# Performance work log

Hardware: AMD Instinct MI355X
Metric: run time of the kernel (lower is better)

## Reference

```python
import jax, jax.numpy as jnp
import numpy as np

N = 4096
IN_DIM = 128
OUT_DIM = 64
LEAKY_SLOPE = 0.2


def setup_inputs() -> dict:
    key = jax.random.key(0)
    ks = jax.random.split(key, 8)
    H = jax.random.normal(ks[0], (N, IN_DIM), dtype=jnp.float32)
    # dense 0/1 adjacency per relation (int constants w.r.t. autodiff)
    A_buys = jax.random.randint(ks[1], (N, N), 0, 2, dtype=jnp.int32)
    A_views = jax.random.randint(ks[2], (N, N), 0, 2, dtype=jnp.int32)
    # xavier_uniform for W (stored [in, out]; Wh = H @ W == torch Linear with weight W.T)
    s_w = float(np.sqrt(6.0 / (IN_DIM + OUT_DIM)))
    W_buys = jax.random.uniform(ks[3], (IN_DIM, OUT_DIM), jnp.float32, -s_w, s_w)
    W_views = jax.random.uniform(ks[4], (IN_DIM, OUT_DIM), jnp.float32, -s_w, s_w)
    # xavier_uniform on a.view(1, 2*out_dim)
    s_a = float(np.sqrt(6.0 / (1 + 2 * OUT_DIM)))
    a_buys = jax.random.uniform(ks[5], (2 * OUT_DIM,), jnp.float32, -s_a, s_a)
    a_views = jax.random.uniform(ks[6], (2 * OUT_DIM,), jnp.float32, -s_a, s_a)
    bias = jnp.zeros((OUT_DIM,), dtype=jnp.float32)
    return {"H": H, "A_buys": A_buys, "A_views": A_views,
            "W_buys": W_buys, "W_views": W_views,
            "a_buys": a_buys, "a_views": a_views, "bias": bias}


def _relation(H, A, W, a):
    Wh = H @ W                                  # [N, OUT]
    # (cat(Wh_i, Wh_j) * a).sum(-1) == Wh_i @ a[:OUT] + Wh_j @ a[OUT:]
    s_i = Wh @ a[:OUT_DIM]                      # [N]
    s_j = Wh @ a[OUT_DIM:]                      # [N]
    e = jax.nn.leaky_relu(s_i[:, None] + s_j[None, :], LEAKY_SLOPE)  # [N, N]
    e = jnp.where(A == 0, -jnp.inf, e)
    alpha = jnp.nan_to_num(jax.nn.softmax(e, axis=1))                # isolated rows -> 0
    return alpha @ Wh                           # [N, OUT]


def reference(H, A_buys, A_views, W_buys, W_views, a_buys, a_views, bias):
    agg = _relation(H, A_buys, W_buys, a_buys) + _relation(H, A_views, W_views, a_views)
    return agg + bias
```

## Files before the change

kernel.cpp:

```cpp
#include <hip/hip_runtime.h>

#define NN 4096
#define IND 128
#define OUTD 64
#define WJ 128
#define NWIN 8
#define LOG2E 1.44269504088896340736f

typedef __attribute__((ext_vector_type(4))) float  floatx4;
typedef __attribute__((ext_vector_type(8))) __bf16 bf16x8;
typedef __attribute__((ext_vector_type(4))) int    intx4;

#if __has_builtin(__builtin_amdgcn_exp2f)
#define EXP2(x) __builtin_amdgcn_exp2f(x)
#else
#define EXP2(x) exp2f(x)
#endif

__device__ __forceinline__ unsigned short f2bf(float f) {
  unsigned int u = __float_as_uint(f);
  u += 0x7fffu + ((u >> 16) & 1u);
  return (unsigned short)(u >> 16);
}

__global__ __launch_bounds__(256) void gat_prep(
    const float* __restrict__ H,
    const float* __restrict__ W0, const float* __restrict__ W1,
    const float* __restrict__ av0, const float* __restrict__ av1,
    unsigned short* __restrict__ whF,
    float* __restrict__ sA, float* __restrict__ sB)
{
  const int rel = blockIdx.y;
  const float* __restrict__ W  = rel ? W1 : W0;
  const float* __restrict__ av = rel ? av1 : av0;
  const int i0 = blockIdx.x * 16;
  const int t = threadIdx.x;
  const int c = t & 63;
  const int wv = __builtin_amdgcn_readfirstlane(t >> 6);
  const float* __restrict__ hp = H + (size_t)(i0 + wv * 4) * IND;

  float acc0 = 0.f, acc1 = 0.f, acc2 = 0.f, acc3 = 0.f;
#pragma unroll 8
  for (int k = 0; k < IND; k += 4) {
    float4 h0 = *(const float4*)(hp + k);
    float4 h1 = *(const float4*)(hp + IND + k);
    float4 h2 = *(const float4*)(hp + 2 * IND + k);
    float4 h3 = *(const float4*)(hp + 3 * IND + k);
    float w0 = W[(k + 0) * OUTD + c];
    float w1 = W[(k + 1) * OUTD + c];
    float w2 = W[(k + 2) * OUTD + c];
    float w3 = W[(k + 3) * OUTD + c];
    acc0 += h0.x * w0 + h0.y * w1 + h0.z * w2 + h0.w * w3;
    acc1 += h1.x * w0 + h1.y * w1 + h1.z * w2 + h1.w * w3;
    acc2 += h2.x * w0 + h2.y * w1 + h2.z * w2 + h2.w * w3;
    acc3 += h3.x * w0 + h3.y * w1 + h3.z * w2 + h3.w * w3;
  }

  const float alo = av[c] * LOG2E, ahi = av[OUTD + c] * LOG2E;
  float pa0 = acc0 * alo, pa1 = acc1 * alo, pa2 = acc2 * alo, pa3 = acc3 * alo;
  float pb0 = acc0 * ahi, pb1 = acc1 * ahi, pb2 = acc2 * ahi, pb3 = acc3 * ahi;
#pragma unroll
  for (int off = 32; off >= 1; off >>= 1) {
    pa0 += __shfl_xor(pa0, off); pa1 += __shfl_xor(pa1, off);
    pa2 += __shfl_xor(pa2, off); pa3 += __shfl_xor(pa3, off);
    pb0 += __shfl_xor(pb0, off); pb1 += __shfl_xor(pb1, off);
    pb2 += __shfl_xor(pb2, off); pb3 += __shfl_xor(pb3, off);
  }
  const int ibase = i0 + wv * 4;
  if (c == 0) {
    float* sa = sA + rel * NN + ibase;
    float* sb = sB + rel * NN + ibase;
    sa[0] = pa0; sa[1] = pa1; sa[2] = pa2; sa[3] = pa3;
    sb[0] = pb0; sb[1] = pb1; sb[2] = pb2; sb[3] = pb3;
  }

  unsigned long long packed =
      (unsigned long long)f2bf(acc0)        | ((unsigned long long)f2bf(acc1) << 16) |
      ((unsigned long long)f2bf(acc2) << 32) | ((unsigned long long)f2bf(acc3) << 48);
  *(unsigned long long*)(whF + ((size_t)(rel * 512 + (ibase >> 3)) * 64 + c) * 8 + (ibase & 7)) = packed;
}

__global__ __launch_bounds__(256, 2) void gat_fused(
    const int* __restrict__ A0, const int* __restrict__ A1,
    const unsigned short* __restrict__ whF,
    const float* __restrict__ sA, const float* __restrict__ sB,
    float* __restrict__ numer,
    float* __restrict__ denom)
{
  __shared__ char lds[4][2][4096];
  const int rel  = blockIdx.y;
  const int i0   = blockIdx.x * 16;
  const int t    = threadIdx.x;
  const int w    = t >> 6;
  const int lane = t & 63;
  const int quad = lane >> 4;
  const int m    = lane & 15;
  const int lj   = lane & 31;
  const int half = lane >> 5;
  const int s_st = lj >> 1;
  const int wboff = s_st * 256 + (lj & 1) * 8;
  const int* __restrict__ A = rel ? A1 : A0;
  const unsigned short* __restrict__ wh = whF + (size_t)rel * 512 * 64 * 8;
  const float* __restrict__ sbp = sB + rel * NN;

  const float siv = sA[rel * NN + i0 + m];
  const int jbase = w * (NWIN * WJ);

  floatx4 acc0 = {0.f,0.f,0.f,0.f}, acc1 = acc0, acc2 = acc0, acc3 = acc0, acc4 = acc0;
  bf16x8 vone;
#pragma unroll
  for (int k = 0; k < 8; k++) vone[k] = (__bf16)1.0f;

  intx4  av2[2][8];
  float4 sjv2[2];
  bf16x8 b[4][4];

  auto issueA = [&](int win) {
    const int jw = jbase + win * WJ;
    const int buf = win & 1;
    sjv2[buf] = *(const float4*)(sbp + jw + lj * 4);
    const int* pA = A + (size_t)(i0 + half) * NN + jw + lj * 4;
#pragma unroll
    for (int p = 0; p < 8; p++)
      av2[buf][p] = __builtin_nontemporal_load((const intx4*)(pA + (size_t)(2 * p) * NN));
  };

  auto stage = [&](int win) {
    const int buf = win & 1;
    char* slice = lds[w][buf];
    const float4 sjv = sjv2[buf];
#pragma unroll
    for (int p = 0; p < 8; p++) {
      const int rp = 2 * p + half;
      const float si = __shfl(siv, rp);
      float t0 = si + sjv.x, t1 = si + sjv.y, t2 = si + sjv.z, t3 = si + sjv.w;
      float e0 = EXP2(fmaxf(t0, 0.2f * t0));
      float e1 = EXP2(fmaxf(t1, 0.2f * t1));
      float e2 = EXP2(fmaxf(t2, 0.2f * t2));
      float e3 = EXP2(fmaxf(t3, 0.2f * t3));
      const intx4 a4 = av2[buf][p];
      e0 = a4[0] ? e0 : 0.f;
      e1 = a4[1] ? e1 : 0.f;
      e2 = a4[2] ? e2 : 0.f;
      e3 = a4[3] ? e3 : 0.f;
      uint2 pk;
      pk.x = (unsigned)f2bf(e0) | ((unsigned)f2bf(e1) << 16);
      pk.y = (unsigned)f2bf(e2) | ((unsigned)f2bf(e3) << 16);
      *(uint2*)(slice + wboff + ((rp ^ s_st) & 15) * 16) = pk;
    }
  };

  auto issueB = [&](int win) {
    const int jw = jbase + win * WJ;
    const unsigned short* bb = wh + ((size_t)(jw >> 3) + quad) * 512 + (size_t)m * 8;
#pragma unroll
    for (int ks = 0; ks < 4; ks++)
#pragma unroll
      for (int nt = 0; nt < 4; nt++)
        b[ks][nt] = *(const bf16x8*)(bb + (size_t)ks * 2048 + nt * 128);
  };

  auto domfma = [&](int win) {
    char* slice = lds[w][win & 1];
    bf16x8 afr[4];
#pragma unroll
    for (int ks = 0; ks < 4; ks++) {
      const int s = ks * 4 + quad;
      afr[ks] = *(const bf16x8*)(slice + s * 256 + ((m ^ s) & 15) * 16);
    }
#pragma unroll
    for (int ks = 0; ks < 4; ks++) {
      acc0 = __builtin_amdgcn_mfma_f32_16x16x32_bf16(afr[ks], b[ks][0], acc0, 0, 0, 0);
      acc1 = __builtin_amdgcn_mfma_f32_16x16x32_bf16(afr[ks], b[ks][1], acc1, 0, 0, 0);
      acc2 = __builtin_amdgcn_mfma_f32_16x16x32_bf16(afr[ks], b[ks][2], acc2, 0, 0, 0);
      acc3 = __builtin_amdgcn_mfma_f32_16x16x32_bf16(afr[ks], b[ks][3], acc3, 0, 0, 0);
      acc4 = __builtin_amdgcn_mfma_f32_16x16x32_bf16(afr[ks], vone,     acc4, 0, 0, 0);
    }
  };

  issueA(0);
  stage(0);
  issueA(1);

#pragma unroll
  for (int win = 0; win < NWIN; win++) {
    issueB(win);
    if (win + 2 < NWIN) issueA(win + 2);
    if (win + 1 < NWIN) stage(win + 1);
    domfma(win);
  }

  float* redw  = (float*)lds[w][0];
  float* dredw = (float*)lds[w][1];
#pragma unroll
  for (int r = 0; r < 4; r++) {
    const int row = quad * 4 + r;
    redw[row * 64 + 0 * 16 + m] = acc0[r];
    redw[row * 64 + 1 * 16 + m] = acc1[r];
    redw[row * 64 + 2 * 16 + m] = acc2[r];
    redw[row * 64 + 3 * 16 + m] = acc3[r];
  }
  if (m == 0) {
#pragma unroll
    for (int r = 0; r < 4; r++) dredw[quad * 4 + r] = acc4[r];
  }
  __syncthreads();

  const int c  = t & 63;
  const int r0 = t >> 6;
  const size_t base = (size_t)rel * NN;
#pragma unroll
  for (int rr = r0; rr < 16; rr += 4) {
    float nsum = 0.f, ds = 0.f;
#pragma unroll
    for (int ww = 0; ww < 4; ww++) {
      nsum += ((const float*)lds[ww][0])[rr * 64 + c];
      ds   += ((const float*)lds[ww][1])[rr];
    }
    numer[(base + i0 + rr) * OUTD + c] = nsum;
    if (c == 0) denom[base + i0 + rr] = ds;
  }
}

__global__ __launch_bounds__(256) void gat_combine(
    const float* __restrict__ numer, const float* __restrict__ denom,
    const float* __restrict__ bias, float* __restrict__ out)
{
  const int idx = blockIdx.x * 256 + threadIdx.x;
  const int i  = idx >> 4;
  const int c4 = idx & 15;
  const float4* nv = (const float4*)numer;

  float4 o = ((const float4*)bias)[c4];
#pragma unroll
  for (int rel = 0; rel < 2; rel++) {
    const size_t base = (size_t)rel * NN + i;
    float4 n = nv[base * 16 + c4];
    float  d = denom[base];
    float inv = d > 0.f ? 1.f / d : 0.f;
    o.x += n.x * inv; o.y += n.y * inv; o.z += n.z * inv; o.w += n.w * inv;
  }
  ((float4*)out)[idx] = o;
}

extern "C" void kernel_launch(void* const* d_in, const int* in_sizes, int n_in,
                              void* d_out, int out_size, void* d_ws, size_t ws_size,
                              hipStream_t stream) {
  const float* H    = (const float*)d_in[0];
  const int*   A0   = (const int*)d_in[1];
  const int*   A1   = (const int*)d_in[2];
  const float* W0   = (const float*)d_in[3];
  const float* W1   = (const float*)d_in[4];
  const float* av0  = (const float*)d_in[5];
  const float* av1  = (const float*)d_in[6];
  const float* bias = (const float*)d_in[7];
  float* out = (float*)d_out;

  const size_t whF_b = (size_t)2 * 512 * 64 * 8 * 2;
  const size_t s_b   = (size_t)2 * NN * 4;

  unsigned short* whF   = (unsigned short*)d_ws;
  float*          sA    = (float*)((char*)d_ws + whF_b);
  float*          sB    = (float*)((char*)d_ws + whF_b + s_b);
  float*          numer = (float*)((char*)d_ws + whF_b + 2 * s_b);
  float*          denom = numer + (size_t)2 * NN * OUTD;

  gat_prep<<<dim3(NN / 16, 2), 256, 0, stream>>>(H, W0, W1, av0, av1, whF, sA, sB);
  gat_fused<<<dim3(NN / 16, 2), 256, 0, stream>>>(A0, A1, whF, sA, sB, numer, denom);
  gat_combine<<<(NN * OUTD / 4) / 256, 256, 0, stream>>>(numer, denom, bias, out);
}
```

Measured before the change: 178.9 us.

## Cut register pressure: bitmask adjacency, split B fragment loads, raise occupancy

Raises the launch bound from 2 to 4 blocks per SIMD. To fit that, it compresses the prefetched adjacency vectors into a 32-bit bitmask per window instead of holding two windows of int4 registers. It also halves the B-fragment register buffer by loading and issuing the MFMAs in two k-halves. The aim is higher occupancy to hide global-memory latency. The cost is less prefetch lookahead for B, extra bit-pack instructions, and possible spills if the tighter register cap is not met.

```diff
diff --git a/kernel.cpp b/kernel.cpp
--- a/kernel.cpp
+++ b/kernel.cpp
@@ -80,7 +80,7 @@
   *(unsigned long long*)(whF + ((size_t)(rel * 512 + (ibase >> 3)) * 64 + c) * 8 + (ibase & 7)) = packed;
 }
 
-__global__ __launch_bounds__(256, 2) void gat_fused(
+__global__ __launch_bounds__(256, 4) void gat_fused(
     const int* __restrict__ A0, const int* __restrict__ A1,
     const unsigned short* __restrict__ whF,
     const float* __restrict__ sA, const float* __restrict__ sB,
@@ -111,38 +111,51 @@
 #pragma unroll
   for (int k = 0; k < 8; k++) vone[k] = (__bf16)1.0f;
 
-  intx4  av2[2][8];
-  float4 sjv2[2];
-  bf16x8 b[4][4];
+  intx4    atr[8];
+  unsigned maskw[2];
+  float4   sjv2[2];
+  bf16x8   b[2][4];
 
   auto issueA = [&](int win) {
     const int jw = jbase + win * WJ;
-    const int buf = win & 1;
-    sjv2[buf] = *(const float4*)(sbp + jw + lj * 4);
+    sjv2[win & 1] = *(const float4*)(sbp + jw + lj * 4);
     const int* pA = A + (size_t)(i0 + half) * NN + jw + lj * 4;
 #pragma unroll
     for (int p = 0; p < 8; p++)
-      av2[buf][p] = __builtin_nontemporal_load((const intx4*)(pA + (size_t)(2 * p) * NN));
+      atr[p] = __builtin_nontemporal_load((const intx4*)(pA + (size_t)(2 * p) * NN));
+  };
+
+  auto packA = [&](int win) {
+    unsigned mk = 0;
+#pragma unroll
+    for (int p = 0; p < 8; p++) {
+      mk |= (atr[p][0] ? 1u : 0u) << (4 * p);
+      mk |= (atr[p][1] ? 2u : 0u) << (4 * p);
+      mk |= (atr[p][2] ? 4u : 0u) << (4 * p);
+      mk |= (atr[p][3] ? 8u : 0u) << (4 * p);
+    }
+    maskw[win & 1] = mk;
   };
 
   auto stage = [&](int win) {
     const int buf = win & 1;
     char* slice = lds[w][buf];
     const float4 sjv = sjv2[buf];
+    const unsigned mk = maskw[buf];
 #pragma unroll
     for (int p = 0; p < 8; p++) {
       const int rp = 2 * p + half;
       const float si = __shfl(siv, rp);
+      const unsigned nib = mk >> (4 * p);
       float t0 = si + sjv.x, t1 = si + sjv.y, t2 = si + sjv.z, t3 = si + sjv.w;
       float e0 = EXP2(fmaxf(t0, 0.2f * t0));
       float e1 = EXP2(fmaxf(t1, 0.2f * t1));
       float e2 = EXP2(fmaxf(t2, 0.2f * t2));
       float e3 = EXP2(fmaxf(t3, 0.2f * t3));
-      const intx4 a4 = av2[buf][p];
-      e0 = a4[0] ? e0 : 0.f;
-      e1 = a4[1] ? e1 : 0.f;
-      e2 = a4[2] ? e2 : 0.f;
-      e3 = a4[3] ? e3 : 0.f;
+      e0 = (nib & 1u) ? e0 : 0.f;
+      e1 = (nib & 2u) ? e1 : 0.f;
+      e2 = (nib & 4u) ? e2 : 0.f;
+      e3 = (nib & 8u) ? e3 : 0.f;
       uint2 pk;
       pk.x = (unsigned)f2bf(e0) | ((unsigned)f2bf(e1) << 16);
       pk.y = (unsigned)f2bf(e2) | ((unsigned)f2bf(e3) << 16);
@@ -150,44 +163,46 @@
     }
   };
 
-  auto issueB = [&](int win) {
+  auto issueB = [&](int win, int h) {
     const int jw = jbase + win * WJ;
     const unsigned short* bb = wh + ((size_t)(jw >> 3) + quad) * 512 + (size_t)m * 8;
 #pragma unroll
-    for (int ks = 0; ks < 4; ks++)
+    for (int k2 = 0; k2 < 2; k2++)
 #pragma unroll
       for (int nt = 0; nt < 4; nt++)
-        b[ks][nt] = *(const bf16x8*)(bb + (size_t)ks * 2048 + nt * 128);
-  };
-
-  auto domfma = [&](int win) {
+        b[k2][nt] = *(const bf16x8*)(bb + (size_t)(2 * h + k2) * 2048 + nt * 128);
+  };
+
+  auto domfma = [&](int win, int h) {
     char* slice = lds[w][win & 1];
-    bf16x8 afr[4];
-#pragma unroll
-    for (int ks = 0; ks < 4; ks++) {
-      const int s = ks * 4 + quad;
-      afr[ks] = *(const bf16x8*)(slice + s * 256 + ((m ^ s) & 15) * 16);
-    }
-#pragma unroll
-    for (int ks = 0; ks < 4; ks++) {
-      acc0 = __builtin_amdgcn_mfma_f32_16x16x32_bf16(afr[ks], b[ks][0], acc0, 0, 0, 0);
-      acc1 = __builtin_amdgcn_mfma_f32_16x16x32_bf16(afr[ks], b[ks][1], acc1, 0, 0, 0);
-      acc2 = __builtin_amdgcn_mfma_f32_16x16x32_bf16(afr[ks], b[ks][2], acc2, 0, 0, 0);
-      acc3 = __builtin_amdgcn_mfma_f32_16x16x32_bf16(afr[ks], b[ks][3], acc3, 0, 0, 0);
-      acc4 = __builtin_amdgcn_mfma_f32_16x16x32_bf16(afr[ks], vone,     acc4, 0, 0, 0);
-    }
-  };
-
-  issueA(0);
-  stage(0);
-  issueA(1);
+    bf16x8 afr[2];
+#pragma unroll
+    for (int k2 = 0; k2 < 2; k2++) {
+      const int s = (2 * h + k2) * 4 + quad;
+      afr[k2] = *(const bf16x8*)(slice + s * 256 + ((m ^ s) & 15) * 16);
+    }
+#pragma unroll
+    for (int k2 = 0; k2 < 2; k2++) {
+      acc0 = __builtin_amdgcn_mfma_f32_16x16x32_bf16(afr[k2], b[k2][0], acc0, 0, 0, 0);
+      acc1 = __builtin_amdgcn_mfma_f32_16x16x32_bf16(afr[k2], b[k2][1], acc1, 0, 0, 0);
+      acc2 = __builtin_amdgcn_mfma_f32_16x16x32_bf16(afr[k2], b[k2][2], acc2, 0, 0, 0);
+      acc3 = __builtin_amdgcn_mfma_f32_16x16x32_bf16(afr[k2], b[k2][3], acc3, 0, 0, 0);
+      acc4 = __builtin_amdgcn_mfma_f32_16x16x32_bf16(afr[k2], vone,     acc4, 0, 0, 0);
+    }
+  };
+
+  issueA(0); packA(0);
+  issueA(1); stage(0); packA(1);
 
 #pragma unroll
   for (int win = 0; win < NWIN; win++) {
-    issueB(win);
+    issueB(win, 0);
     if (win + 2 < NWIN) issueA(win + 2);
     if (win + 1 < NWIN) stage(win + 1);
-    domfma(win);
+    domfma(win, 0);
+    issueB(win, 1);
+    domfma(win, 1);
+    if (win + 2 < NWIN) packA(win + 2);
   }
 
   float* redw  = (float*)lds[w][0];
```

Result: slower. 188.8 us (+5.6%).
